# Kernel optimization log

Measured on AMD Instinct MI355X. Metric: run time of the kernel, lower is better.

The kernel has to match this reference:

```python
import jax, jax.numpy as jnp
import numpy as np

INPT, HID, NNODE, K, B = 64, 128, 10000, 16, 8

def setup_inputs() -> dict:
    key = jax.random.key(0)
    ks = jax.random.split(key, 12)
    def lin(k, fan_in, fan_out):
        # orthogonal-ish init stand-in; exact init values are irrelevant for the reference math
        return jax.random.normal(k, (fan_in, fan_out), jnp.float32) / np.sqrt(fan_in)
    return {
        "state": jax.random.normal(ks[0], (B, NNODE, INPT), jnp.float32),
        "internal": jax.random.normal(ks[1], (B, NNODE, INPT), jnp.float32),
        "state_neigh": jax.random.randint(ks[2], (NNODE, K), 0, NNODE),
        "internal_neigh": jax.random.randint(ks[3], (NNODE, K), 0, NNODE),
        "W1": lin(ks[4], INPT, HID), "b1": jnp.zeros((HID,), jnp.float32),
        "W2": lin(ks[5], HID, HID), "b2": jnp.zeros((HID,), jnp.float32),
        "Wu1": lin(ks[6], 2 * HID, HID), "bu1": jnp.zeros((HID,), jnp.float32),
        "Wu2": lin(ks[7], 2 * HID, HID), "bu2": jnp.zeros((HID,), jnp.float32),
    }

def _aggregate(se, ie, s_idx, i_idx):
    # se, ie: [B, N, H]; idx: [N, K] -> gather neighbors and sum over K
    g_s = jnp.take(se, s_idx, axis=1).sum(axis=2)   # [B, N, H]
    g_i = jnp.take(ie, i_idx, axis=1).sum(axis=2)   # [B, N, H]
    return g_s + g_i

def _update(aggr, h, W, b):
    x = jnp.concatenate((aggr, h), axis=-1)          # [B, N, 2H]
    return jax.nn.relu(x @ W + b)

def reference(state, internal, state_neigh, internal_neigh,
              W1, b1, W2, b2, Wu1, bu1, Wu2, bu2):
    # layer-1 embeddings
    state_embed = jax.nn.relu(state @ W1 + b1)       # [B, N, H]
    internal_embed = jax.nn.relu(internal @ W1 + b1)
    aggr1 = _aggregate(state_embed, internal_embed, state_neigh, internal_neigh)
    hu1 = _update(aggr1, internal_embed, Wu1, bu1)   # [B, N, H]
    # layer-2 embeddings
    se2 = jax.nn.relu(state_embed @ W2 + b2)
    ie2 = jax.nn.relu(hu1 @ W2 + b2)
    aggr2 = _aggregate(se2, ie2, state_neigh, internal_neigh)
    hu2 = _update(aggr2, ie2, Wu2, bu2)              # [B, N, H]
    return hu1, hu2
```

## Files before the change

### kernel.cpp

```cpp
#include <hip/hip_runtime.h>

#define HID 128
#define NNODE 10000
#define KN 16
#define ROWS 80000
#define NCHUNK 157

typedef __attribute__((ext_vector_type(8))) short short8;
typedef __attribute__((ext_vector_type(4))) float f32x4;
typedef __attribute__((ext_vector_type(2))) float f32x2;
typedef __attribute__((ext_vector_type(4))) unsigned int u32x4;

__device__ __forceinline__ unsigned short f2b(float f) {
    unsigned u = __float_as_uint(f);
    u += 0x7FFFu + ((u >> 16) & 1u);
    return (unsigned short)(u >> 16);
}

__global__ __launch_bounds__(256) void wconv_all(
    const float* __restrict__ W1, const float* __restrict__ W2,
    const float* __restrict__ Wu1, const float* __restrict__ Wu2,
    unsigned short* __restrict__ W1t, unsigned short* __restrict__ W2t,
    unsigned short* __restrict__ Wu1t, unsigned short* __restrict__ Wu2t) {
    int idx = blockIdx.x * 256 + threadIdx.x;
    const float* W; unsigned short* Wt; int K; int off;
    if (idx < 8192)       { W = W1;  Wt = W1t;  K = 64;  off = idx; }
    else if (idx < 24576) { W = W2;  Wt = W2t;  K = 128; off = idx - 8192; }
    else if (idx < 57344) { W = Wu1; Wt = Wu1t; K = 256; off = idx - 24576; }
    else                  { W = Wu2; Wt = Wu2t; K = 256; off = idx - 57344; }
    int n = off & 127, k = off >> 7;
    Wt[n * K + k] = f2b(W[off]);
}

template<int K, bool AF32>
__global__ __launch_bounds__(256) void embed_mfma(
    const void* __restrict__ A0, const void* __restrict__ A1,
    const unsigned short* __restrict__ Wt, const float* __restrict__ bias,
    unsigned short* __restrict__ Y0, unsigned short* __restrict__ Y1) {
    int g = blockIdx.x;
    const void* Ain = A0; unsigned short* Yb = Y0;
    if (g >= 1250) { Ain = A1; Yb = Y1; g -= 1250; }

    const int wave = threadIdx.x >> 6, lane = threadIdx.x & 63;
    const int lrow = lane & 15, lk = lane >> 4;
    const int m0 = g * 64 + wave * 16;
    const int arow = m0 + lrow;

    short8 a[K / 32];
    if constexpr (AF32) {
        const float* A = (const float*)Ain;
#pragma unroll
        for (int kt = 0; kt < K / 32; ++kt) {
            const float* p = A + (size_t)arow * K + kt * 32 + lk * 8;
            f32x4 f0 = *(const f32x4*)p;
            f32x4 f1 = *(const f32x4*)(p + 4);
            short8 v;
#pragma unroll
            for (int e = 0; e < 4; ++e) { v[e] = (short)f2b(f0[e]); v[4 + e] = (short)f2b(f1[e]); }
            a[kt] = v;
        }
    } else {
        const unsigned short* A = (const unsigned short*)Ain;
#pragma unroll
        for (int kt = 0; kt < K / 32; ++kt)
            a[kt] = *(const short8*)(A + (size_t)arow * K + kt * 32 + lk * 8);
    }

#pragma unroll
    for (int nt = 0; nt < 8; ++nt) {
        f32x4 acc = {0.f, 0.f, 0.f, 0.f};
#pragma unroll
        for (int kt = 0; kt < K / 32; ++kt) {
            short8 b = *(const short8*)(Wt + (nt * 16 + lrow) * K + kt * 32 + lk * 8);
            acc = __builtin_amdgcn_mfma_f32_16x16x32_bf16(a[kt], b, acc, 0, 0, 0);
        }
        const int ocol = nt * 16 + lrow;
        const float bv = bias[ocol];
#pragma unroll
        for (int j = 0; j < 4; ++j) {
            const int orow = m0 + lk * 4 + j;
            float v = acc[j] + bv;
            v = v > 0.f ? v : 0.f;
            Yb[(size_t)orow * HID + ocol] = f2b(v);
        }
    }
}

__global__ __launch_bounds__(512) void aggr_kernel(
    const unsigned short* __restrict__ SE, const unsigned short* __restrict__ IE,
    const int* __restrict__ sidx, const int* __restrict__ iidx,
    unsigned short* __restrict__ G) {
    __shared__ int sh_idx[64][33];
    const int t = threadIdx.x;
    const int b = blockIdx.x & 7;
    const int hc = blockIdx.x >> 3;
    const int h = hc >= NCHUNK ? 1 : 0;
    const int c = hc - h * NCHUNK;
    const int n0 = c * 64;

#pragma unroll
    for (int q = 0; q < 4; ++q) {
        const int e = t + q * 512;
        const int r = e >> 5, k = e & 31;
        int nr = n0 + r; if (nr > NNODE - 1) nr = NNODE - 1;
        sh_idx[r][k] = (k < KN) ? sidx[nr * KN + k] : iidx[nr * KN + (k - KN)];
    }
    __syncthreads();

    const int r = t >> 3, p = t & 7;
    const int col0 = h * 64 + p * 8;
    const int n = n0 + r;
    const size_t base = (size_t)b * NNODE * HID + col0;

    f32x2 acc[4];
#pragma unroll
    for (int w = 0; w < 4; ++w) acc[w] = (f32x2){0.f, 0.f};

#pragma unroll
    for (int q = 0; q < 4; ++q) {
        const unsigned short* P = (q < 2) ? SE : IE;
        u32x4 vals[8];
#pragma unroll
        for (int j = 0; j < 8; ++j)
            vals[j] = *(const u32x4*)(P + base + (size_t)sh_idx[r][q * 8 + j] * HID);
#pragma unroll
        for (int j = 0; j < 8; ++j)
#pragma unroll
            for (int w = 0; w < 4; ++w) {
                const unsigned u = vals[j][w];
                acc[w] += (f32x2){__uint_as_float(u << 16), __uint_as_float(u & 0xffff0000u)};
            }
    }

    if (n < NNODE) {
        short8 ov;
#pragma unroll
        for (int w = 0; w < 4; ++w) {
            ov[2 * w]     = (short)f2b(acc[w].x);
            ov[2 * w + 1] = (short)f2b(acc[w].y);
        }
        *(short8*)(G + ((size_t)b * NNODE + n) * HID + col0) = ov;
    }
}

__global__ __launch_bounds__(512) void update_gemm(
    const unsigned short* __restrict__ G, const unsigned short* __restrict__ H,
    const unsigned short* __restrict__ Wut, const float* __restrict__ bu,
    float* __restrict__ Yf, unsigned short* __restrict__ Yb, int writeb) {
    const int t = threadIdx.x, wave = t >> 6, lane = t & 63;
    const int lrow = lane & 15, lk = lane >> 4;
    const int rs = wave & 1, colg = wave >> 1;
    const int m0 = blockIdx.x * 64 + rs * 32;
    const int row0 = m0 + lrow, row1 = m0 + 16 + lrow;

    short8 a0[8], a1[8];
#pragma unroll
    for (int kt = 0; kt < 4; ++kt) {
        a0[kt]     = *(const short8*)(G + (size_t)row0 * HID + kt * 32 + lk * 8);
        a1[kt]     = *(const short8*)(G + (size_t)row1 * HID + kt * 32 + lk * 8);
        a0[4 + kt] = *(const short8*)(H + (size_t)row0 * HID + kt * 32 + lk * 8);
        a1[4 + kt] = *(const short8*)(H + (size_t)row1 * HID + kt * 32 + lk * 8);
    }

#pragma unroll
    for (int nt2 = 0; nt2 < 2; ++nt2) {
        const int nt = colg * 2 + nt2;
        f32x4 acc0 = {0.f, 0.f, 0.f, 0.f};
        f32x4 acc1 = {0.f, 0.f, 0.f, 0.f};
#pragma unroll
        for (int kt = 0; kt < 8; ++kt) {
            short8 bb = *(const short8*)(Wut + (nt * 16 + lrow) * 256 + kt * 32 + lk * 8);
            acc0 = __builtin_amdgcn_mfma_f32_16x16x32_bf16(a0[kt], bb, acc0, 0, 0, 0);
            acc1 = __builtin_amdgcn_mfma_f32_16x16x32_bf16(a1[kt], bb, acc1, 0, 0, 0);
        }
        const int ocol = nt * 16 + lrow;
        const float bv = bu[ocol];
#pragma unroll
        for (int j = 0; j < 4; ++j) {
            const size_t r0 = (size_t)m0 + lk * 4 + j;
            const size_t r1 = r0 + 16;
            float v0 = acc0[j] + bv; v0 = v0 > 0.f ? v0 : 0.f;
            float v1 = acc1[j] + bv; v1 = v1 > 0.f ? v1 : 0.f;
            Yf[r0 * HID + ocol] = v0;
            Yf[r1 * HID + ocol] = v1;
            if (writeb) {
                Yb[r0 * HID + ocol] = f2b(v0);
                Yb[r1 * HID + ocol] = f2b(v1);
            }
        }
    }
}

extern "C" void kernel_launch(void* const* d_in, const int* in_sizes, int n_in,
                              void* d_out, int out_size, void* d_ws, size_t ws_size,
                              hipStream_t stream) {
    const float* state    = (const float*)d_in[0];
    const float* internal = (const float*)d_in[1];
    const int*   sidx     = (const int*)d_in[2];
    const int*   iidx     = (const int*)d_in[3];
    const float* W1  = (const float*)d_in[4];
    const float* b1  = (const float*)d_in[5];
    const float* W2  = (const float*)d_in[6];
    const float* b2  = (const float*)d_in[7];
    const float* Wu1 = (const float*)d_in[8];
    const float* bu1 = (const float*)d_in[9];
    const float* Wu2 = (const float*)d_in[10];
    const float* bu2 = (const float*)d_in[11];

    float* hu1 = (float*)d_out;
    float* hu2 = hu1 + (size_t)ROWS * HID;

    unsigned short* W1t  = (unsigned short*)d_ws;
    unsigned short* W2t  = W1t  + 64 * 128;
    unsigned short* Wu1t = W2t  + 128 * 128;
    unsigned short* Wu2t = Wu1t + 256 * 128;
    unsigned short* bufA = Wu2t + 256 * 128;
    unsigned short* bufB = bufA + (size_t)ROWS * HID;
    unsigned short* bufC = bufB + (size_t)ROWS * HID;
    unsigned short* bufD = bufC + (size_t)ROWS * HID;

    const size_t need4 = (size_t)90112 * 2 + 4 * (size_t)ROWS * HID * 2;
    const bool big = ws_size >= need4;

    dim3 b256(256), b512(512);
    const int AGRID = 8 * 2 * NCHUNK;

    wconv_all<<<352, b256, 0, stream>>>(W1, W2, Wu1, Wu2, W1t, W2t, Wu1t, Wu2t);

    embed_mfma<64, true><<<2500, b256, 0, stream>>>(state, internal, W1t, b1, bufA, bufB);

    if (big) {
        aggr_kernel<<<AGRID, b512, 0, stream>>>(bufA, bufB, sidx, iidx, bufD);
        update_gemm<<<1250, b512, 0, stream>>>(bufD, bufB, Wu1t, bu1, hu1, bufC, 1);
        embed_mfma<128, false><<<2500, b256, 0, stream>>>(bufA, bufC, W2t, b2, bufB, bufD);
        aggr_kernel<<<AGRID, b512, 0, stream>>>(bufB, bufD, sidx, iidx, bufA);
        update_gemm<<<1250, b512, 0, stream>>>(bufA, bufD, Wu2t, bu2, hu2, nullptr, 0);
    } else {
        unsigned short* Ghu2 = (unsigned short*)hu2;
        aggr_kernel<<<AGRID, b512, 0, stream>>>(bufA, bufB, sidx, iidx, Ghu2);
        update_gemm<<<1250, b512, 0, stream>>>(Ghu2, bufB, Wu1t, bu1, hu1, bufC, 1);
        embed_mfma<128, false><<<1250, b256, 0, stream>>>(bufA, nullptr, W2t, b2, bufB, nullptr);
        embed_mfma<128, false><<<1250, b256, 0, stream>>>(bufC, nullptr, W2t, b2, bufA, nullptr);
        aggr_kernel<<<AGRID, b512, 0, stream>>>(bufB, bufA, sidx, iidx, bufC);
        update_gemm<<<1250, b512, 0, stream>>>(bufC, bufA, Wu2t, bu2, hu2, nullptr, 0);
    }
}
```

Before: 250.2 us.

## Swap MFMA operands for vectorized stores and hoist weight fragments into registers

```diff
diff --git a/kernel.cpp b/kernel.cpp
--- a/kernel.cpp
+++ b/kernel.cpp
@@ -5,11 +5,13 @@
 #define KN 16
 #define ROWS 80000
 #define NCHUNK 157
+#define NTILES 2500
 
 typedef __attribute__((ext_vector_type(8))) short short8;
 typedef __attribute__((ext_vector_type(4))) float f32x4;
 typedef __attribute__((ext_vector_type(2))) float f32x2;
 typedef __attribute__((ext_vector_type(4))) unsigned int u32x4;
+typedef __attribute__((ext_vector_type(2))) unsigned int u32x2;
 
 __device__ __forceinline__ unsigned short f2b(float f) {
     unsigned u = __float_as_uint(f);
@@ -33,56 +35,79 @@
 }
 
 template<int K, bool AF32>
-__global__ __launch_bounds__(256) void embed_mfma(
+__global__ __launch_bounds__(512) void embed2(
     const void* __restrict__ A0, const void* __restrict__ A1,
     const unsigned short* __restrict__ Wt, const float* __restrict__ bias,
-    unsigned short* __restrict__ Y0, unsigned short* __restrict__ Y1) {
-    int g = blockIdx.x;
-    const void* Ain = A0; unsigned short* Yb = Y0;
-    if (g >= 1250) { Ain = A1; Yb = Y1; g -= 1250; }
-
-    const int wave = threadIdx.x >> 6, lane = threadIdx.x & 63;
+    unsigned short* __restrict__ Y0, unsigned short* __restrict__ Y1, int tot) {
+    const int t = threadIdx.x, w = t >> 6, lane = t & 63;
     const int lrow = lane & 15, lk = lane >> 4;
-    const int m0 = g * 64 + wave * 16;
-    const int arow = m0 + lrow;
-
-    short8 a[K / 32];
-    if constexpr (AF32) {
-        const float* A = (const float*)Ain;
-#pragma unroll
-        for (int kt = 0; kt < K / 32; ++kt) {
-            const float* p = A + (size_t)arow * K + kt * 32 + lk * 8;
-            f32x4 f0 = *(const f32x4*)p;
-            f32x4 f1 = *(const f32x4*)(p + 4);
-            short8 v;
-#pragma unroll
-            for (int e = 0; e < 4; ++e) { v[e] = (short)f2b(f0[e]); v[4 + e] = (short)f2b(f1[e]); }
-            a[kt] = v;
-        }
-    } else {
-        const unsigned short* A = (const unsigned short*)Ain;
+    const int rs = w & 1, ng = w >> 1;
+    const int col0 = ng * 32;
+
+    short8 wf[2][K / 32];
+    f32x4 bv[2];
+#pragma unroll
+    for (int p = 0; p < 2; ++p) {
+        bv[p] = *(const f32x4*)(bias + col0 + p * 16 + lk * 4);
 #pragma unroll
         for (int kt = 0; kt < K / 32; ++kt)
-            a[kt] = *(const short8*)(A + (size_t)arow * K + kt * 32 + lk * 8);
-    }
-
-#pragma unroll
-    for (int nt = 0; nt < 8; ++nt) {
-        f32x4 acc = {0.f, 0.f, 0.f, 0.f};
-#pragma unroll
-        for (int kt = 0; kt < K / 32; ++kt) {
-            short8 b = *(const short8*)(Wt + (nt * 16 + lrow) * K + kt * 32 + lk * 8);
-            acc = __builtin_amdgcn_mfma_f32_16x16x32_bf16(a[kt], b, acc, 0, 0, 0);
-        }
-        const int ocol = nt * 16 + lrow;
-        const float bv = bias[ocol];
-#pragma unroll
-        for (int j = 0; j < 4; ++j) {
-            const int orow = m0 + lk * 4 + j;
-            float v = acc[j] + bv;
-            v = v > 0.f ? v : 0.f;
-            Yb[(size_t)orow * HID + ocol] = f2b(v);
-        }
+            wf[p][kt] = *(const short8*)(Wt + (col0 + p * 16 + lrow) * K + kt * 32 + lk * 8);
+    }
+
+    int T = blockIdx.x;
+    if (T >= tot) return;
+
+    auto loadx = [&](int TT, short8* xf) {
+        const int half = TT >= NTILES;
+        const void* A = half ? A1 : A0;
+        const int row = (TT - half * NTILES) * 32 + rs * 16 + lrow;
+        if constexpr (AF32) {
+            const float* X = (const float*)A + (size_t)row * K;
+#pragma unroll
+            for (int kt = 0; kt < K / 32; ++kt) {
+                f32x4 f0 = *(const f32x4*)(X + kt * 32 + lk * 8);
+                f32x4 f1 = *(const f32x4*)(X + kt * 32 + lk * 8 + 4);
+                short8 v;
+#pragma unroll
+                for (int e = 0; e < 4; ++e) { v[e] = (short)f2b(f0[e]); v[4 + e] = (short)f2b(f1[e]); }
+                xf[kt] = v;
+            }
+        } else {
+            const unsigned short* X = (const unsigned short*)A + (size_t)row * K;
+#pragma unroll
+            for (int kt = 0; kt < K / 32; ++kt)
+                xf[kt] = *(const short8*)(X + kt * 32 + lk * 8);
+        }
+    };
+
+    short8 xf[K / 32], xn[K / 32];
+    loadx(T, xf);
+    for (;;) {
+        const int Tn = T + gridDim.x;
+        const bool more = Tn < tot;
+        if (more) loadx(Tn, xn);
+
+        const int half = T >= NTILES;
+        unsigned short* Y = half ? Y1 : Y0;
+        const int row = (T - half * NTILES) * 32 + rs * 16 + lrow;
+#pragma unroll
+        for (int p = 0; p < 2; ++p) {
+            f32x4 acc = {0.f, 0.f, 0.f, 0.f};
+#pragma unroll
+            for (int kt = 0; kt < K / 32; ++kt)
+                acc = __builtin_amdgcn_mfma_f32_16x16x32_bf16(wf[p][kt], xf[kt], acc, 0, 0, 0);
+            float v0 = acc[0] + bv[p][0]; v0 = v0 > 0.f ? v0 : 0.f;
+            float v1 = acc[1] + bv[p][1]; v1 = v1 > 0.f ? v1 : 0.f;
+            float v2 = acc[2] + bv[p][2]; v2 = v2 > 0.f ? v2 : 0.f;
+            float v3 = acc[3] + bv[p][3]; v3 = v3 > 0.f ? v3 : 0.f;
+            u32x2 ov = {(unsigned)f2b(v0) | ((unsigned)f2b(v1) << 16),
+                        (unsigned)f2b(v2) | ((unsigned)f2b(v3) << 16)};
+            *(u32x2*)(Y + (size_t)row * HID + col0 + p * 16 + lk * 4) = ov;
+        }
+        if (!more) break;
+#pragma unroll
+        for (int kt = 0; kt < K / 32; ++kt) xf[kt] = xn[kt];
+        T = Tn;
     }
 }
 
@@ -143,49 +168,50 @@
     }
 }
 
-__global__ __launch_bounds__(512) void update_gemm(
+__global__ __launch_bounds__(512) void update_gemm2(
     const unsigned short* __restrict__ G, const unsigned short* __restrict__ H,
     const unsigned short* __restrict__ Wut, const float* __restrict__ bu,
     float* __restrict__ Yf, unsigned short* __restrict__ Yb, int writeb) {
-    const int t = threadIdx.x, wave = t >> 6, lane = t & 63;
+    const int t = threadIdx.x, w = t >> 6, lane = t & 63;
     const int lrow = lane & 15, lk = lane >> 4;
-    const int rs = wave & 1, colg = wave >> 1;
-    const int m0 = blockIdx.x * 64 + rs * 32;
-    const int row0 = m0 + lrow, row1 = m0 + 16 + lrow;
-
-    short8 a0[8], a1[8];
-#pragma unroll
-    for (int kt = 0; kt < 4; ++kt) {
-        a0[kt]     = *(const short8*)(G + (size_t)row0 * HID + kt * 32 + lk * 8);
-        a1[kt]     = *(const short8*)(G + (size_t)row1 * HID + kt * 32 + lk * 8);
-        a0[4 + kt] = *(const short8*)(H + (size_t)row0 * HID + kt * 32 + lk * 8);
-        a1[4 + kt] = *(const short8*)(H + (size_t)row1 * HID + kt * 32 + lk * 8);
-    }
-
-#pragma unroll
-    for (int nt2 = 0; nt2 < 2; ++nt2) {
-        const int nt = colg * 2 + nt2;
-        f32x4 acc0 = {0.f, 0.f, 0.f, 0.f};
-        f32x4 acc1 = {0.f, 0.f, 0.f, 0.f};
-#pragma unroll
-        for (int kt = 0; kt < 8; ++kt) {
-            short8 bb = *(const short8*)(Wut + (nt * 16 + lrow) * 256 + kt * 32 + lk * 8);
-            acc0 = __builtin_amdgcn_mfma_f32_16x16x32_bf16(a0[kt], bb, acc0, 0, 0, 0);
-            acc1 = __builtin_amdgcn_mfma_f32_16x16x32_bf16(a1[kt], bb, acc1, 0, 0, 0);
-        }
-        const int ocol = nt * 16 + lrow;
-        const float bv = bu[ocol];
-#pragma unroll
-        for (int j = 0; j < 4; ++j) {
-            const size_t r0 = (size_t)m0 + lk * 4 + j;
-            const size_t r1 = r0 + 16;
-            float v0 = acc0[j] + bv; v0 = v0 > 0.f ? v0 : 0.f;
-            float v1 = acc1[j] + bv; v1 = v1 > 0.f ? v1 : 0.f;
-            Yf[r0 * HID + ocol] = v0;
-            Yf[r1 * HID + ocol] = v1;
+    const int rs = w & 1, ng = w >> 1;
+    const int col0 = ng * 32;
+
+    short8 wf[2][8];
+    f32x4 bv[2];
+#pragma unroll
+    for (int p = 0; p < 2; ++p) {
+        bv[p] = *(const f32x4*)(bu + col0 + p * 16 + lk * 4);
+#pragma unroll
+        for (int kt = 0; kt < 8; ++kt)
+            wf[p][kt] = *(const short8*)(Wut + (col0 + p * 16 + lrow) * 256 + kt * 32 + lk * 8);
+    }
+
+    for (int T = blockIdx.x; T < NTILES; T += gridDim.x) {
+        const int row = T * 32 + rs * 16 + lrow;
+        short8 xf[8];
+#pragma unroll
+        for (int kt = 0; kt < 4; ++kt) {
+            xf[kt]     = *(const short8*)(G + (size_t)row * HID + kt * 32 + lk * 8);
+            xf[4 + kt] = *(const short8*)(H + (size_t)row * HID + kt * 32 + lk * 8);
+        }
+#pragma unroll
+        for (int p = 0; p < 2; ++p) {
+            f32x4 acc = {0.f, 0.f, 0.f, 0.f};
+#pragma unroll
+            for (int kt = 0; kt < 8; ++kt)
+                acc = __builtin_amdgcn_mfma_f32_16x16x32_bf16(wf[p][kt], xf[kt], acc, 0, 0, 0);
+            f32x4 o;
+#pragma unroll
+            for (int j = 0; j < 4; ++j) {
+                float v = acc[j] + bv[p][j];
+                o[j] = v > 0.f ? v : 0.f;
+            }
+            *(f32x4*)(Yf + (size_t)row * HID + col0 + p * 16 + lk * 4) = o;
             if (writeb) {
-                Yb[r0 * HID + ocol] = f2b(v0);
-                Yb[r1 * HID + ocol] = f2b(v1);
+                u32x2 ov = {(unsigned)f2b(o[0]) | ((unsigned)f2b(o[1]) << 16),
+                            (unsigned)f2b(o[2]) | ((unsigned)f2b(o[3]) << 16)};
+                *(u32x2*)(Yb + (size_t)row * HID + col0 + p * 16 + lk * 4) = ov;
             }
         }
     }
@@ -227,21 +253,21 @@
 
     wconv_all<<<352, b256, 0, stream>>>(W1, W2, Wu1, Wu2, W1t, W2t, Wu1t, Wu2t);
 
-    embed_mfma<64, true><<<2500, b256, 0, stream>>>(state, internal, W1t, b1, bufA, bufB);
+    embed2<64, true><<<1250, b512, 0, stream>>>(state, internal, W1t, b1, bufA, bufB, 2 * NTILES);
 
     if (big) {
         aggr_kernel<<<AGRID, b512, 0, stream>>>(bufA, bufB, sidx, iidx, bufD);
-        update_gemm<<<1250, b512, 0, stream>>>(bufD, bufB, Wu1t, bu1, hu1, bufC, 1);
-        embed_mfma<128, false><<<2500, b256, 0, stream>>>(bufA, bufC, W2t, b2, bufB, bufD);
+        update_gemm2<<<1250, b512, 0, stream>>>(bufD, bufB, Wu1t, bu1, hu1, bufC, 1);
+        embed2<128, false><<<1250, b512, 0, stream>>>(bufA, bufC, W2t, b2, bufB, bufD, 2 * NTILES);
         aggr_kernel<<<AGRID, b512, 0, stream>>>(bufB, bufD, sidx, iidx, bufA);
-        update_gemm<<<1250, b512, 0, stream>>>(bufA, bufD, Wu2t, bu2, hu2, nullptr, 0);
+        update_gemm2<<<1250, b512, 0, stream>>>(bufA, bufD, Wu2t, bu2, hu2, nullptr, 0);
     } else {
         unsigned short* Ghu2 = (unsigned short*)hu2;
         aggr_kernel<<<AGRID, b512, 0, stream>>>(bufA, bufB, sidx, iidx, Ghu2);
-        update_gemm<<<1250, b512, 0, stream>>>(Ghu2, bufB, Wu1t, bu1, hu1, bufC, 1);
-        embed_mfma<128, false><<<1250, b256, 0, stream>>>(bufA, nullptr, W2t, b2, bufB, nullptr);
-        embed_mfma<128, false><<<1250, b256, 0, stream>>>(bufC, nullptr, W2t, b2, bufA, nullptr);
+        update_gemm2<<<1250, b512, 0, stream>>>(Ghu2, bufB, Wu1t, bu1, hu1, bufC, 1);
+        embed2<128, false><<<1250, b512, 0, stream>>>(bufA, nullptr, W2t, b2, bufB, nullptr, NTILES);
+        embed2<128, false><<<1250, b512, 0, stream>>>(bufC, nullptr, W2t, b2, bufA, nullptr, NTILES);
         aggr_kernel<<<AGRID, b512, 0, stream>>>(bufB, bufA, sidx, iidx, bufC);
-        update_gemm<<<1250, b512, 0, stream>>>(bufC, bufA, Wu2t, bu2, hu2, nullptr, 0);
-    }
-}
+        update_gemm2<<<1250, b512, 0, stream>>>(bufC, bufA, Wu2t, bu2, hu2, nullptr, 0);
+    }
+}
```

Measured after the change: 231.9 us. -7.3%, faster.
